# Performance work log

Measured on AMD Instinct MI355X. Metric: run time of the kernel, lower is better.

The kernel has to match this reference:

```python
import jax, jax.numpy as jnp
import numpy as np
import math

D_MODEL = 768
NUM_HEADS = 12
D_K = D_MODEL // NUM_HEADS

def setup_inputs() -> dict:
    key = jax.random.key(0)
    k_x, k_q, k_k, k_v, k_o = jax.random.split(key, 5)
    x = jax.random.normal(k_x, (2, 2048, D_MODEL), dtype=jnp.float32)
    std = math.sqrt(2.0 / (D_MODEL + D_MODEL))
    # trunc_normal approx: clip normal to [-3std, 3std]
    def tn(k):
        return jnp.clip(jax.random.normal(k, (D_MODEL, D_MODEL), dtype=jnp.float32) * std, -3 * std, 3 * std)
    return {
        "x": x,
        "weight_query": tn(k_q),
        "weight_key": tn(k_k),
        "weight_value": tn(k_v),
        "weight_output": tn(k_o),
    }

def reference(x, weight_query, weight_key, weight_value, weight_output):
    # x: (b, s, d_model); weights: (d_out, d_model)
    b, s, _ = x.shape
    def proj_heads(w):
        y = jnp.einsum('od,bsd->bso', w, x)  # (b, s, h*dk)
        return y.reshape(b, s, NUM_HEADS, D_K).transpose(0, 2, 1, 3)  # (b, h, s, dk)
    Q = proj_heads(weight_query)
    K = proj_heads(weight_key)
    V = proj_heads(weight_value)
    scores = jnp.einsum('bhqd,bhkd->bhqk', Q, K) / jnp.sqrt(jnp.asarray(D_K, x.dtype))
    causal = jnp.tril(jnp.ones((s, s), dtype=bool))  # (sq, sk)
    scores = jnp.where(causal, scores, -jnp.inf)
    attn = jax.nn.softmax(scores, axis=-1)
    out_heads = jnp.einsum('bhqk,bhkd->bhqd', attn, V)  # (b, h, s, dv)
    attn_out = out_heads.transpose(0, 2, 1, 3).reshape(b, s, NUM_HEADS * D_K)
    return jnp.einsum('di,bsi->bsd', weight_output, attn_out)
```

## Files before the change

### kernel.cpp

```cpp
#include <hip/hip_runtime.h>
#include <stdint.h>

typedef float f32x4 __attribute__((ext_vector_type(4)));
typedef __bf16 bf16x8 __attribute__((ext_vector_type(8)));
typedef uint32_t u32a  __attribute__((may_alias));
typedef uint2    u2a   __attribute__((may_alias));
typedef uint4    u4a   __attribute__((may_alias));

#define VS 2064

__device__ __forceinline__ ushort f2b(float f) {
  uint32_t u = __builtin_bit_cast(uint32_t, f);
  u += 0x7FFFu + ((u >> 16) & 1u);
  return (ushort)(u >> 16);
}
__device__ __forceinline__ uint32_t b16(uint32_t u) {
  u += 0x7FFFu + ((u >> 16) & 1u);
  return u >> 16;
}
__device__ __forceinline__ float blo(uint32_t a) {
  return __builtin_bit_cast(float, a << 16);
}
__device__ __forceinline__ float bhi(uint32_t a) {
  return __builtin_bit_cast(float, a & 0xFFFF0000u);
}

__device__ __forceinline__ bf16x8 ld_frag(const ushort* p) {
  u4a u = *(const u4a*)p;
  return __builtin_bit_cast(bf16x8, u);
}

__device__ __forceinline__ u4a cvt8(const float* p) {
  u4a a = *(const u4a*)p, b = *(const u4a*)(p + 4), o;
  o.x = b16(a.x) | (b16(a.y) << 16);
  o.y = b16(a.z) | (b16(a.w) << 16);
  o.z = b16(b.x) | (b16(b.y) << 16);
  o.w = b16(b.z) | (b16(b.w) << 16);
  return o;
}

__device__ __forceinline__ void load_lds16(const void* g, void* l) {
  __builtin_amdgcn_global_load_lds(
      (const __attribute__((address_space(1))) uint32_t*)g,
      (__attribute__((address_space(3))) uint32_t*)l, 16, 0, 0);
}

__global__ __launch_bounds__(256) void convert_kernel(
    const float* __restrict__ x,  const float* __restrict__ wq,
    const float* __restrict__ wk, const float* __restrict__ wv,
    const float* __restrict__ wo,
    ushort* __restrict__ xb,  ushort* __restrict__ wqb,
    ushort* __restrict__ wkb, ushort* __restrict__ wvb,
    ushort* __restrict__ wob)
{
  const size_t NX = 3145728, NW = 589824;
  size_t idx = ((size_t)blockIdx.x * 256 + threadIdx.x) * 8;
  const float* src; ushort* dst; size_t off;
  if      (idx < NX)          { src = x;  dst = xb;  off = idx; }
  else if (idx < NX + NW)     { src = wq; dst = wqb; off = idx - NX; }
  else if (idx < NX + 2 * NW) { src = wk; dst = wkb; off = idx - NX - NW; }
  else if (idx < NX + 3 * NW) { src = wv; dst = wvb; off = idx - NX - 2 * NW; }
  else                        { src = wo; dst = wob; off = idx - NX - 3 * NW; }
  *(u4a*)(dst + off) = cvt8(src + off);
}

__global__ __launch_bounds__(256) void gemm_qkv(
    const ushort* __restrict__ A,
    const ushort* __restrict__ B0, const ushort* __restrict__ B1,
    const ushort* __restrict__ B2,
    ushort* __restrict__ Qo, ushort* __restrict__ Ko, ushort* __restrict__ Vt,
    int M, int N, int K)
{
  const ushort* B = blockIdx.z == 0 ? B0 : (blockIdx.z == 1 ? B1 : B2);
  const int m0 = blockIdx.x * 128, n0 = blockIdx.y * 64;
  __shared__ ushort As[128 * 64];
  __shared__ ushort Bs[64 * 64];
  const int tid = threadIdx.x, wave = tid >> 6, lane = tid & 63;
  const int quad = lane >> 4, l16 = lane & 15;
  const int mw = (wave & 1) * 64, nw = (wave >> 1) * 32;
  f32x4 acc[4][2] = {};

  for (int k0 = 0; k0 < K; k0 += 64) {
#pragma unroll
    for (int i = 0; i < 4; ++i) {
      int c = i * 256 + tid;
      load_lds16(A + (size_t)(m0 + (c >> 3)) * K + k0 + (c & 7) * 8,
                 As + (size_t)(i * 256 + wave * 64) * 8);
    }
#pragma unroll
    for (int i = 0; i < 2; ++i) {
      int c = i * 256 + tid;
      load_lds16(B + (size_t)(n0 + (c >> 3)) * K + k0 + (c & 7) * 8,
                 Bs + (size_t)(i * 256 + wave * 64) * 8);
    }
    __syncthreads();
#pragma unroll
    for (int ks = 0; ks < 2; ++ks) {
      bf16x8 af[4], bfr[2];
#pragma unroll
      for (int i = 0; i < 4; ++i)
        af[i]  = ld_frag(As + (mw + i * 16 + l16) * 64 + ks * 32 + quad * 8);
#pragma unroll
      for (int j = 0; j < 2; ++j)
        bfr[j] = ld_frag(Bs + (nw + j * 16 + l16) * 64 + ks * 32 + quad * 8);
#pragma unroll
      for (int i = 0; i < 4; ++i)
#pragma unroll
        for (int j = 0; j < 2; ++j)
          acc[i][j] = __builtin_amdgcn_mfma_f32_16x16x32_bf16(af[i], bfr[j], acc[i][j], 0, 0, 0);
    }
    __syncthreads();
  }
  if (blockIdx.z < 2) {
    ushort* C = blockIdx.z == 0 ? Qo : Ko;
    const float sc = blockIdx.z == 0 ? 0.18033688f : 1.0f;
#pragma unroll
    for (int i = 0; i < 4; ++i)
#pragma unroll
      for (int j = 0; j < 2; ++j)
#pragma unroll
        for (int r = 0; r < 4; ++r) {
          int row = m0 + mw + i * 16 + quad * 4 + r;
          int col = n0 + nw + j * 16 + l16;
          C[(size_t)row * N + col] = f2b(acc[i][j][r] * sc);
        }
  } else {
#pragma unroll
    for (int i = 0; i < 4; ++i)
#pragma unroll
      for (int j = 0; j < 2; ++j) {
        int col = n0 + nw + j * 16 + l16;
        int h = col >> 6, dv = col & 63;
        int t = m0 + mw + i * 16 + quad * 4;
        int b = t >> 11, s = t & 2047;
        u2a pw;
        pw.x = (uint32_t)f2b(acc[i][j][0]) | ((uint32_t)f2b(acc[i][j][1]) << 16);
        pw.y = (uint32_t)f2b(acc[i][j][2]) | ((uint32_t)f2b(acc[i][j][3]) << 16);
        *(u2a*)(Vt + (((size_t)b * 12 + h) * 64 + dv) * VS + s) = pw;
      }
  }
}

__global__ __launch_bounds__(256) void gemm_out(
    const ushort* __restrict__ A, const ushort* __restrict__ B,
    float* __restrict__ C, int M, int N, int K)
{
  const int m0 = blockIdx.x * 64, n0 = blockIdx.y * 64;
  __shared__ ushort As[64 * 64];
  __shared__ ushort Bs[64 * 64];
  const int tid = threadIdx.x, wave = tid >> 6, lane = tid & 63;
  const int quad = lane >> 4, l16 = lane & 15;
  const int mw = (wave & 1) * 32, nw = (wave >> 1) * 32;
  f32x4 acc[2][2] = {};

  for (int k0 = 0; k0 < K; k0 += 64) {
#pragma unroll
    for (int i = 0; i < 2; ++i) {
      int c = i * 256 + tid;
      load_lds16(A + (size_t)(m0 + (c >> 3)) * K + k0 + (c & 7) * 8,
                 As + (size_t)(i * 256 + wave * 64) * 8);
      load_lds16(B + (size_t)(n0 + (c >> 3)) * K + k0 + (c & 7) * 8,
                 Bs + (size_t)(i * 256 + wave * 64) * 8);
    }
    __syncthreads();
#pragma unroll
    for (int ks = 0; ks < 2; ++ks) {
      bf16x8 af[2], bfr[2];
#pragma unroll
      for (int i = 0; i < 2; ++i)
        af[i]  = ld_frag(As + (mw + i * 16 + l16) * 64 + ks * 32 + quad * 8);
#pragma unroll
      for (int j = 0; j < 2; ++j)
        bfr[j] = ld_frag(Bs + (nw + j * 16 + l16) * 64 + ks * 32 + quad * 8);
#pragma unroll
      for (int i = 0; i < 2; ++i)
#pragma unroll
        for (int j = 0; j < 2; ++j)
          acc[i][j] = __builtin_amdgcn_mfma_f32_16x16x32_bf16(af[i], bfr[j], acc[i][j], 0, 0, 0);
    }
    __syncthreads();
  }
#pragma unroll
  for (int i = 0; i < 2; ++i)
#pragma unroll
    for (int j = 0; j < 2; ++j)
#pragma unroll
      for (int r = 0; r < 4; ++r) {
        int row = m0 + mw + i * 16 + quad * 4 + r;
        int col = n0 + nw + j * 16 + l16;
        C[(size_t)row * N + col] = acc[i][j][r];
      }
}

__global__ __launch_bounds__(256) void attn_kernel(
    const ushort* __restrict__ Qb, const ushort* __restrict__ Kb,
    const ushort* __restrict__ Vt, ushort* __restrict__ Opart,
    float* __restrict__ Lp)
{
  const int S = 2048, DM = 768;
  const int fid = blockIdx.x;
  const int nf  = (fid & 7) * 192 + (fid >> 3);
  const int grp = nf >> 6;
  const int wit = nf & 63;
  const int bb = grp / 12, h = grp % 12;
  const int pair = wit >> 2, j = wit & 3;

  const ushort* Qp  = Qb + (size_t)bb * S * DM + h * 64;
  const ushort* Kp  = Kb + (size_t)bb * S * DM + h * 64;
  const ushort* Vth = Vt + ((size_t)bb * 12 + h) * 64 * VS;

  __shared__ ushort Ks[64 * 72];
  __shared__ ushort Vs[64 * 72];

  const int tid = threadIdx.x, wave = tid >> 6, lane = tid & 63;
  const int quad = lane >> 4, l16 = lane & 15;
  const float NEG_BIG = -1.0e30f;

  const int qtA = pair, qtB = 31 - pair;
  const int qgA = qtA * 64 + wave * 16 + l16;
  const int qgB = qtB * 64 + wave * 16 + l16;

  bf16x8 bqA0 = ld_frag(Qp + (size_t)qgA * DM + quad * 8);
  bf16x8 bqA1 = ld_frag(Qp + (size_t)qgA * DM + 32 + quad * 8);
  bf16x8 bqB0 = ld_frag(Qp + (size_t)qgB * DM + quad * 8);
  bf16x8 bqB1 = ld_frag(Qp + (size_t)qgB * DM + 32 + quad * 8);

  u4a one4; one4.x = one4.y = one4.z = one4.w = 0x3F803F80u;
  const bf16x8 ones = __builtin_bit_cast(bf16x8, one4);

  f32x4 accA[4] = {}, accB[4] = {};
  f32x4 alA = {}, alB = {};

  for (int kt = j; kt <= qtB; kt += 4) {
    const int kk0 = kt * 64;
#pragma unroll
    for (int i = 0; i < 2; ++i) {
      int c = i * 256 + tid;
      int r = c >> 3, col = (c & 7) * 8;
      *(u4a*)(Ks + r * 72 + col) = *(const u4a*)(Kp + (size_t)(kk0 + r) * DM + col);
    }
#pragma unroll
    for (int i = 0; i < 2; ++i) {
      int c = i * 256 + tid;
      int dv = c >> 3, kc8 = c & 7;
      u4a g = *(const u4a*)(Vth + (size_t)dv * VS + kk0 + kc8 * 8);
      int pos = ((kc8 >> 2) * 32) + ((kc8 & 1) * 16) + (((kc8 >> 1) & 1) * 4);
      u2a lo, hi;
      lo.x = g.x; lo.y = g.y; hi.x = g.z; hi.y = g.w;
      *(u2a*)(Vs + dv * 72 + pos)     = lo;
      *(u2a*)(Vs + dv * 72 + pos + 8) = hi;
    }
    __syncthreads();

    auto strip = [&](const bf16x8& bq0, const bf16x8& bq1, f32x4* acc_o,
                     f32x4& acc_l, int qg, bool domask) {
      f32x4 sacc[4] = {};
#pragma unroll
      for (int tt = 0; tt < 4; ++tt) {
        bf16x8 ak0 = ld_frag(Ks + (tt * 16 + l16) * 72 + quad * 8);
        bf16x8 ak1 = ld_frag(Ks + (tt * 16 + l16) * 72 + 32 + quad * 8);
        sacc[tt] = __builtin_amdgcn_mfma_f32_16x16x32_bf16(ak0, bq0, sacc[tt], 0, 0, 0);
        sacc[tt] = __builtin_amdgcn_mfma_f32_16x16x32_bf16(ak1, bq1, sacc[tt], 0, 0, 0);
      }
      if (domask) {
#pragma unroll
        for (int tt = 0; tt < 4; ++tt)
#pragma unroll
          for (int r = 0; r < 4; ++r) {
            int kkg = kk0 + tt * 16 + quad * 4 + r;
            if (kkg > qg) sacc[tt][r] = NEG_BIG;
          }
      }
#pragma unroll
      for (int g = 0; g < 2; ++g) {
        u4a pu;
        {
          int tt = g * 2;
          uint32_t u0 = __builtin_bit_cast(uint32_t, exp2f(sacc[tt][0]));
          uint32_t u1 = __builtin_bit_cast(uint32_t, exp2f(sacc[tt][1]));
          uint32_t u2 = __builtin_bit_cast(uint32_t, exp2f(sacc[tt][2]));
          uint32_t u3 = __builtin_bit_cast(uint32_t, exp2f(sacc[tt][3]));
          pu.x = __builtin_amdgcn_perm(u1, u0, 0x07060302u);
          pu.y = __builtin_amdgcn_perm(u3, u2, 0x07060302u);
          u0 = __builtin_bit_cast(uint32_t, exp2f(sacc[tt + 1][0]));
          u1 = __builtin_bit_cast(uint32_t, exp2f(sacc[tt + 1][1]));
          u2 = __builtin_bit_cast(uint32_t, exp2f(sacc[tt + 1][2]));
          u3 = __builtin_bit_cast(uint32_t, exp2f(sacc[tt + 1][3]));
          pu.z = __builtin_amdgcn_perm(u1, u0, 0x07060302u);
          pu.w = __builtin_amdgcn_perm(u3, u2, 0x07060302u);
        }
        bf16x8 ap = __builtin_bit_cast(bf16x8, pu);
        acc_l = __builtin_amdgcn_mfma_f32_16x16x32_bf16(ap, ones, acc_l, 0, 0, 0);
#pragma unroll
        for (int ct = 0; ct < 4; ++ct) {
          bf16x8 bv = ld_frag(Vs + (size_t)(ct * 16 + l16) * 72 + g * 32 + quad * 8);
          acc_o[ct] = __builtin_amdgcn_mfma_f32_16x16x32_bf16(ap, bv, acc_o[ct], 0, 0, 0);
        }
      }
    };

    strip(bqB0, bqB1, accB, alB, qgB, kt == qtB);
    if (kt <= qtA)
      strip(bqA0, bqA1, accA, alA, qgA, kt == qtA);
    __syncthreads();
  }

  const int base = ((bb * 12 + h) << 5);
  const int r0 = wave * 16 + quad * 4;
  {
    const int slot = (base + qtB) * 4 + j;
    ushort* Os = Opart + (size_t)slot * 4096;
#pragma unroll
    for (int ct = 0; ct < 4; ++ct) {
      int col = ct * 16 + l16;
      Os[(r0 + 0) * 64 + col] = f2b(accB[ct][0]);
      Os[(r0 + 1) * 64 + col] = f2b(accB[ct][1]);
      Os[(r0 + 2) * 64 + col] = f2b(accB[ct][2]);
      Os[(r0 + 3) * 64 + col] = f2b(accB[ct][3]);
    }
    if (l16 == 0) {
#pragma unroll
      for (int r = 0; r < 4; ++r)
        Lp[(size_t)slot * 64 + r0 + r] = alB[r];
    }
  }
  {
    const int slot = (base + qtA) * 4 + j;
    ushort* Os = Opart + (size_t)slot * 4096;
#pragma unroll
    for (int ct = 0; ct < 4; ++ct) {
      int col = ct * 16 + l16;
      Os[(r0 + 0) * 64 + col] = f2b(accA[ct][0]);
      Os[(r0 + 1) * 64 + col] = f2b(accA[ct][1]);
      Os[(r0 + 2) * 64 + col] = f2b(accA[ct][2]);
      Os[(r0 + 3) * 64 + col] = f2b(accA[ct][3]);
    }
    if (l16 == 0) {
#pragma unroll
      for (int r = 0; r < 4; ++r)
        Lp[(size_t)slot * 64 + r0 + r] = alA[r];
    }
  }
}

__global__ __launch_bounds__(256) void combine_kernel(
    const ushort* __restrict__ Opart, const float* __restrict__ Lp,
    ushort* __restrict__ Ab, int split)
{
  const int sid = blockIdx.x;
  const int bb = sid / 384, rem = sid % 384, h = rem >> 5, qt = rem & 31;
  const int t = threadIdx.x, row = t >> 2, cg = (t & 3) * 16;
  const float* lp = Lp + (size_t)sid * split * 64 + row;
  float denom = 0.0f;
  for (int i = 0; i < split; ++i) denom += lp[(size_t)i * 64];
  const float inv = 1.0f / denom;
  float os[16] = {};
  const ushort* p0 = Opart + (size_t)sid * split * 4096 + row * 64 + cg;
  for (int i = 0; i < split; ++i) {
#pragma unroll
    for (int g = 0; g < 2; ++g) {
      u4a a = *(const u4a*)(p0 + (size_t)i * 4096 + g * 8);
      os[g * 8 + 0] += blo(a.x); os[g * 8 + 1] += bhi(a.x);
      os[g * 8 + 2] += blo(a.y); os[g * 8 + 3] += bhi(a.y);
      os[g * 8 + 4] += blo(a.z); os[g * 8 + 5] += bhi(a.z);
      os[g * 8 + 6] += blo(a.w); os[g * 8 + 7] += bhi(a.w);
    }
  }
  ushort* dst = Ab + ((size_t)(bb * 2048 + qt * 64 + row)) * 768 + h * 64 + cg;
#pragma unroll
  for (int g = 0; g < 2; ++g) {
    u4a o;
    o.x = (uint32_t)f2b(os[g * 8 + 0] * inv) | ((uint32_t)f2b(os[g * 8 + 1] * inv) << 16);
    o.y = (uint32_t)f2b(os[g * 8 + 2] * inv) | ((uint32_t)f2b(os[g * 8 + 3] * inv) << 16);
    o.z = (uint32_t)f2b(os[g * 8 + 4] * inv) | ((uint32_t)f2b(os[g * 8 + 5] * inv) << 16);
    o.w = (uint32_t)f2b(os[g * 8 + 6] * inv) | ((uint32_t)f2b(os[g * 8 + 7] * inv) << 16);
    *(u4a*)(dst + g * 8) = o;
  }
}

extern "C" void kernel_launch(void* const* d_in, const int* in_sizes, int n_in,
                              void* d_out, int out_size, void* d_ws, size_t ws_size,
                              hipStream_t stream) {
  (void)in_sizes; (void)n_in; (void)out_size; (void)ws_size;
  const float* x  = (const float*)d_in[0];
  const float* wq = (const float*)d_in[1];
  const float* wk = (const float*)d_in[2];
  const float* wv = (const float*)d_in[3];
  const float* wo = (const float*)d_in[4];

  const size_t NT = (size_t)4096 * 768;
  const size_t NW = (size_t)768 * 768;
  const size_t NV = (size_t)24 * 64 * VS;
  ushort* xb    = (ushort*)d_ws;
  ushort* Qbuf  = xb + NT;
  ushort* Kbuf  = Qbuf + NT;
  ushort* Vt    = Kbuf + NT;
  ushort* wqb   = Vt + NV;
  ushort* wkb   = wqb + NW;
  ushort* wvb   = wkb + NW;
  ushort* wob   = wvb + NW;
  ushort* Opart = wob + NW;
  float* Lp     = (float*)(Opart + (size_t)3072 * 4096);
  ushort* Abuf  = xb;

  convert_kernel<<<2688, 256, 0, stream>>>(x, wq, wk, wv, wo,
                                           xb, wqb, wkb, wvb, wob);
  gemm_qkv<<<dim3(32, 12, 3), 256, 0, stream>>>(
      xb, wqb, wkb, wvb, Qbuf, Kbuf, Vt, 4096, 768, 768);
  attn_kernel<<<1536, 256, 0, stream>>>(Qbuf, Kbuf, Vt, Opart, Lp);
  combine_kernel<<<768, 256, 0, stream>>>(Opart, Lp, Abuf, 4);
  gemm_out<<<dim3(64, 12), 256, 0, stream>>>(
      Abuf, wob, (float*)d_out, 4096, 768, 768);
}
```

Baseline: 156.1 us.

## Double the key tile to 128 and load K directly into swizzled LDS

Each iteration now stages 128 keys of K and V instead of 64, and runs up to four strips per barrier pair. The aim is to halve the number of __syncthreads and loop iterations. K is now copied global-to-LDS through load_lds16 into an XOR-swizzled unpadded layout rather than a padded register round-trip. Coarser tiles make the 4-way key split per query pair less balanced, and they double the LDS footprint, which may cut occupancy.

```diff
diff --git a/kernel.cpp b/kernel.cpp
--- a/kernel.cpp
+++ b/kernel.cpp
@@ -209,8 +209,8 @@
   const ushort* Kp  = Kb + (size_t)bb * S * DM + h * 64;
   const ushort* Vth = Vt + ((size_t)bb * 12 + h) * 64 * VS;
 
-  __shared__ ushort Ks[64 * 72];
-  __shared__ ushort Vs[64 * 72];
+  __shared__ ushort Ks[128 * 64];
+  __shared__ ushort Vs[64 * 136];
 
   const int tid = threadIdx.x, wave = tid >> 6, lane = tid & 63;
   const int quad = lane >> 4, l16 = lane & 15;
@@ -231,34 +231,39 @@
   f32x4 accA[4] = {}, accB[4] = {};
   f32x4 alA = {}, alB = {};
 
-  for (int kt = j; kt <= qtB; kt += 4) {
-    const int kk0 = kt * 64;
-#pragma unroll
-    for (int i = 0; i < 2; ++i) {
+  const int kttMax = qtB >> 1;
+  for (int ktt = j; ktt <= kttMax; ktt += 4) {
+    const int kk0 = ktt * 128;
+#pragma unroll
+    for (int i = 0; i < 4; ++i) {
       int c = i * 256 + tid;
-      int r = c >> 3, col = (c & 7) * 8;
-      *(u4a*)(Ks + r * 72 + col) = *(const u4a*)(Kp + (size_t)(kk0 + r) * DM + col);
-    }
-#pragma unroll
-    for (int i = 0; i < 2; ++i) {
+      load_lds16(Kp + (size_t)(kk0 + (c >> 3)) * DM + (((c & 7) ^ ((c >> 3) & 7)) << 3),
+                 Ks + (size_t)(i * 256 + wave * 64) * 8);
+    }
+#pragma unroll
+    for (int i = 0; i < 4; ++i) {
       int c = i * 256 + tid;
-      int dv = c >> 3, kc8 = c & 7;
+      int dv = c >> 4, kc8 = c & 15;
       u4a g = *(const u4a*)(Vth + (size_t)dv * VS + kk0 + kc8 * 8);
       int pos = ((kc8 >> 2) * 32) + ((kc8 & 1) * 16) + (((kc8 >> 1) & 1) * 4);
       u2a lo, hi;
       lo.x = g.x; lo.y = g.y; hi.x = g.z; hi.y = g.w;
-      *(u2a*)(Vs + dv * 72 + pos)     = lo;
-      *(u2a*)(Vs + dv * 72 + pos + 8) = hi;
+      *(u2a*)(Vs + dv * 136 + pos)     = lo;
+      *(u2a*)(Vs + dv * 136 + pos + 8) = hi;
     }
     __syncthreads();
 
     auto strip = [&](const bf16x8& bq0, const bf16x8& bq1, f32x4* acc_o,
-                     f32x4& acc_l, int qg, bool domask) {
+                     f32x4& acc_l, int qg, bool domask, int half) {
+      const int rbase = half * 64, gb = half * 2;
+      const int kk0h = kk0 + half * 64;
+      const int sw = (l16 & 7) << 4;
       f32x4 sacc[4] = {};
 #pragma unroll
       for (int tt = 0; tt < 4; ++tt) {
-        bf16x8 ak0 = ld_frag(Ks + (tt * 16 + l16) * 72 + quad * 8);
-        bf16x8 ak1 = ld_frag(Ks + (tt * 16 + l16) * 72 + 32 + quad * 8);
+        const ushort* krp = Ks + (size_t)(rbase + tt * 16 + l16) * 64;
+        bf16x8 ak0 = ld_frag(krp + (((quad * 16)      ^ sw) >> 1));
+        bf16x8 ak1 = ld_frag(krp + (((64 + quad * 16) ^ sw) >> 1));
         sacc[tt] = __builtin_amdgcn_mfma_f32_16x16x32_bf16(ak0, bq0, sacc[tt], 0, 0, 0);
         sacc[tt] = __builtin_amdgcn_mfma_f32_16x16x32_bf16(ak1, bq1, sacc[tt], 0, 0, 0);
       }
@@ -267,7 +272,7 @@
         for (int tt = 0; tt < 4; ++tt)
 #pragma unroll
           for (int r = 0; r < 4; ++r) {
-            int kkg = kk0 + tt * 16 + quad * 4 + r;
+            int kkg = kk0h + tt * 16 + quad * 4 + r;
             if (kkg > qg) sacc[tt][r] = NEG_BIG;
           }
       }
@@ -293,15 +298,20 @@
         acc_l = __builtin_amdgcn_mfma_f32_16x16x32_bf16(ap, ones, acc_l, 0, 0, 0);
 #pragma unroll
         for (int ct = 0; ct < 4; ++ct) {
-          bf16x8 bv = ld_frag(Vs + (size_t)(ct * 16 + l16) * 72 + g * 32 + quad * 8);
+          bf16x8 bv = ld_frag(Vs + (size_t)(ct * 16 + l16) * 136 + (gb + g) * 32 + quad * 8);
           acc_o[ct] = __builtin_amdgcn_mfma_f32_16x16x32_bf16(ap, bv, acc_o[ct], 0, 0, 0);
         }
       }
     };
 
-    strip(bqB0, bqB1, accB, alB, qgB, kt == qtB);
-    if (kt <= qtA)
-      strip(bqA0, bqA1, accA, alA, qgA, kt == qtA);
+    const int t0 = 2 * ktt, t1 = 2 * ktt + 1;
+    strip(bqB0, bqB1, accB, alB, qgB, t0 == qtB, 0);
+    if (t1 <= qtB)
+      strip(bqB0, bqB1, accB, alB, qgB, t1 == qtB, 1);
+    if (t0 <= qtA)
+      strip(bqA0, bqA1, accA, alA, qgA, t0 == qtA, 0);
+    if (t1 <= qtA)
+      strip(bqA0, bqA1, accA, alA, qgA, t1 == qtA, 1);
     __syncthreads();
   }
 
```

Measured after the change: 159.1 us. About the same (+1.9%).
